# Kernel optimization log

Hardware: AMD Instinct MI355X
Metric: run time of the kernel (lower is better)

## Reference

```python
import math
import jax, jax.numpy as jnp
import numpy as np

B, T, S, C, E = 16, 1024, 1024, 1024, 1024
NORM_C = 0.5


def setup_inputs() -> dict:
    key = jax.random.key(0)
    ks = jax.random.split(key, 9)
    return {
        "x": jax.random.normal(ks[0], (B, T, C), dtype=jnp.float32),
        "target_embedding": jax.random.normal(ks[1], (B, T, E), dtype=jnp.float32),
        "enc_keys": jax.random.normal(ks[2], (B, E, S), dtype=jnp.float32),      # encoder_out[0]
        "enc_values": jax.random.normal(ks[3], (B, S, E), dtype=jnp.float32),    # encoder_out[1]
        "encoder_padding_mask": jax.random.randint(ks[4], (B, S), 0, 2).astype(bool),
        "w_in": jax.random.normal(ks[5], (E, C), dtype=jnp.float32) / np.sqrt(C),
        "b_in": jnp.zeros((E,), dtype=jnp.float32),
        "w_out": jax.random.normal(ks[6], (C, E), dtype=jnp.float32) / np.sqrt(E),
        "b_out": jnp.zeros((C,), dtype=jnp.float32),
    }


def reference(x, target_embedding, enc_keys, enc_values, encoder_padding_mask,
              w_in, b_in, w_out, b_out):
    scale = jnp.float32(math.sqrt(NORM_C))
    residual = x
    # in_projection + target embedding, rescale
    h = (jnp.einsum("btc,ec->bte", x, w_in) + b_in + target_embedding) * scale
    # attention scores: bmm with keys [B,E,S]
    scores = jnp.einsum("bte,bes->bts", h, enc_keys)
    neg_inf = jnp.float32(float("-inf"))
    scores = jnp.where(encoder_padding_mask[:, None, :], neg_inf, scores)
    attn_scores = jax.nn.softmax(scores, axis=-1)
    # weighted sum of values
    ctx = jnp.einsum("bts,bse->bte", attn_scores, enc_values)
    # data-dependent rescale: multiply by sqrt(valid token count)
    s = jnp.float32(S) - jnp.sum(encoder_padding_mask.astype(ctx.dtype), axis=1, keepdims=True)  # [B,1]
    s = s[:, :, None]  # [B,1,1]
    ctx = ctx * (s * jax.lax.rsqrt(s))
    out = (jnp.einsum("bte,ce->btc", ctx, w_out) + b_out + residual) * scale
    return (out, attn_scores)
```

## Files before the change

kernel.cpp:

```cpp
#include <hip/hip_runtime.h>


#define SCALE_F 0.70710678118654752440f

constexpr int BB = 16, TT = 1024, SS = 1024, CC = 1024, EE = 1024;

typedef float    f32x4 __attribute__((ext_vector_type(4)));
typedef _Float16 f16x8 __attribute__((ext_vector_type(8)));
typedef _Float16 f16x4 __attribute__((ext_vector_type(4)));

__device__ __forceinline__ void gload_lds16(const _Float16* g, _Float16* l) {
  __builtin_amdgcn_global_load_lds((const __attribute__((address_space(1))) void*)g,
                                   (__attribute__((address_space(3))) void*)l,
                                   16, 0, 0);
}

__global__ __launch_bounds__(256) void cvt_f16(const float* __restrict__ s,
                                               _Float16* __restrict__ d, long n) {
  long i = ((long)blockIdx.x * 256 + threadIdx.x) * 8;
  if (i >= n) return;
  f32x4 a = *(const f32x4*)(s + i);
  f32x4 b = *(const f32x4*)(s + i + 4);
  f16x8 h;
  h[0]=(_Float16)a[0]; h[1]=(_Float16)a[1]; h[2]=(_Float16)a[2]; h[3]=(_Float16)a[3];
  h[4]=(_Float16)b[0]; h[5]=(_Float16)b[1]; h[6]=(_Float16)b[2]; h[7]=(_Float16)b[3];
  *(f16x8*)(d + i) = h;
}

__global__ __launch_bounds__(256) void transpose_cvt(const float* __restrict__ src,
                                                     _Float16* __restrict__ dst,
                                                     int R, int Cc) {
  __shared__ float tile[64][65];
  const int b = blockIdx.z;
  const int r0 = blockIdx.y * 64, c0 = blockIdx.x * 64;
  const int t = threadIdx.x;
  const int tr = t >> 4, tc4 = (t & 15) * 4;
  const float* s = src + (size_t)b * R * Cc;
#pragma unroll
  for (int i = 0; i < 4; ++i) {
    f32x4 v = *(const f32x4*)(s + (size_t)(r0 + i * 16 + tr) * Cc + c0 + tc4);
    tile[i * 16 + tr][tc4 + 0] = v[0]; tile[i * 16 + tr][tc4 + 1] = v[1];
    tile[i * 16 + tr][tc4 + 2] = v[2]; tile[i * 16 + tr][tc4 + 3] = v[3];
  }
  __syncthreads();
  _Float16* d = dst + (size_t)b * Cc * R;
#pragma unroll
  for (int j = 0; j < 4; ++j) {
    const int cl = j * 16 + tr;
    f16x4 h;
    h[0] = (_Float16)tile[tc4 + 0][cl]; h[1] = (_Float16)tile[tc4 + 1][cl];
    h[2] = (_Float16)tile[tc4 + 2][cl]; h[3] = (_Float16)tile[tc4 + 3][cl];
    *(f16x4*)(d + (size_t)(c0 + cl) * R + r0 + tc4) = h;
  }
}

__global__ __launch_bounds__(256) void mask_prep(const unsigned char* __restrict__ mraw,
                                                 float* __restrict__ maskneg,
                                                 float* __restrict__ sscale) {
  const int b = blockIdx.x, t = threadIdx.x;
  __shared__ int bytemode_sh, cnt_sh;
  if (t == 0) { bytemode_sh = 0; cnt_sh = 0; }
  __syncthreads();
  const unsigned int* mu = (const unsigned int*)mraw;
  int local = 0;
  for (int i = t; i < (BB * SS) / 4; i += 256) {
    unsigned int v = mu[i];
    if (v != 0u && v != 1u && v != 0x3f800000u) local = 1;
  }
  if (local) atomicOr(&bytemode_sh, 1);
  __syncthreads();
  const int bytemode = bytemode_sh;
  int cnt = 0;
  for (int s = t; s < SS; s += 256) {
    int m = bytemode ? (mraw[b * SS + s] != 0) : (mu[b * SS + s] != 0u);
    maskneg[b * SS + s] = m ? -__builtin_inff() : 0.0f;
    cnt += m;
  }
#pragma unroll
  for (int o = 32; o; o >>= 1) cnt += __shfl_down(cnt, o);
  if ((t & 63) == 0) atomicAdd(&cnt_sh, cnt);
  __syncthreads();
  if (t == 0) {
    float sv = (float)SS - (float)cnt_sh;
    sscale[b] = sv * rsqrtf(sv);
  }
}

template <int EPI>
__global__ __launch_bounds__(256, 4)
void gemm_hp(const _Float16* __restrict__ A, const _Float16* __restrict__ Bmat,
             long aStride, long bStride, long oStride,
             int M, int N, int K,
             void* __restrict__ outp,
             const float* __restrict__ bias,
             const void* __restrict__ addmat,
             const float* __restrict__ extra) {
  __shared__ __attribute__((aligned(16))) _Float16 smem[2][8192];

  const int t = threadIdx.x;
  const int lane = t & 63;
  const int wid = t >> 6;
  const int wr = wid >> 1, wc = wid & 1;
  const int z = blockIdx.z;
  const int lo = lane & 15, hi = lane >> 4;
  const int nt = K >> 5;

  const int gx = gridDim.x;
  const int fblk = blockIdx.x + blockIdx.y * gx;
  const int q = (gx * gridDim.y) >> 3;
  const int wg = (fblk & 7) * q + (fblk >> 3);
  const long rowBase = (long)(wg / gx) * 128;
  const long colBase = (long)(wg % gx) * 128;

  const _Float16* Ag = A + (size_t)z * aStride + rowBase * K;
  const _Float16* Bg = Bmat + (size_t)z * bStride + colBase * K;

  const int sP = t >> 3;
  const int sl = (t & 7) ^ (sP & 7);
  const int sh64 = (sl >> 2) * 64;
  const int sc8 = (sl & 3) * 8;

  f32x4 acc[4][4] = {};

  auto stage = [&](int buf, int u) {
    _Float16* base = &smem[buf][0];
    const size_t k0 = (size_t)u * 32 + sc8;
#pragma unroll
    for (int op = 0; op < 2; ++op) {
      const _Float16* g = op ? Bg : Ag;
#pragma unroll
      for (int i = 0; i < 2; ++i) {
        const int gRow = 32 * i + sP + sh64;
        gload_lds16(g + (size_t)gRow * K + k0,
                    base + op * 4096 + i * 2048 + t * 8);
      }
    }
  };

  stage(0, 0);
  asm volatile("s_waitcnt vmcnt(0)" ::: "memory");
  __syncthreads();

  const int aslot = ((4 * wr + hi) ^ (lo & 7)) << 3;
  const int bslot = ((4 * wc + hi) ^ (lo & 7)) << 3;

  for (int u = 0; u < nt; ++u) {
    if (u + 1 < nt) stage((u + 1) & 1, u + 1);
    const _Float16* As = &smem[u & 1][0];
    const _Float16* Bs = &smem[u & 1][4096];
    f16x8 a[4], b[4];
#pragma unroll
    for (int m = 0; m < 4; ++m)
      a[m] = *(const f16x8*)&As[(m * 16 + lo) * 64 + aslot];
#pragma unroll
    for (int n = 0; n < 4; ++n)
      b[n] = *(const f16x8*)&Bs[(n * 16 + lo) * 64 + bslot];
#pragma unroll
    for (int m = 0; m < 4; ++m)
#pragma unroll
      for (int n = 0; n < 4; ++n)
        acc[m][n] = __builtin_amdgcn_mfma_f32_16x16x32_f16(a[m], b[n],
                                                           acc[m][n], 0, 0, 0);
    __syncthreads();
  }

  constexpr int EPS = 68;
  const int fr = lane & 15;
  const int fq = (lane >> 4) * 4;
  const int er = lane >> 2;
  const int ec = (lane & 3) * 16;
  const long gc0 = colBase + wc * 64 + ec;
  float* ep = (float*)&smem[0][0] + wid * (16 * EPS);

  f32x4 biasv[4], maskv[4], av[4];
  float sc = 0.f;
  auto load_add = [&](long gr) {
    if constexpr (EPI == 1) {
      const float* am = (const float*)addmat;
#pragma unroll
      for (int i = 0; i < 4; ++i) av[i] = *(const f32x4*)&am[gr * N + gc0 + i * 4];
    } else if constexpr (EPI == 5) {
      const _Float16* am = (const _Float16*)addmat;
      f16x8 h0 = *(const f16x8*)&am[gr * N + gc0];
      f16x8 h1 = *(const f16x8*)&am[gr * N + gc0 + 8];
#pragma unroll
      for (int i = 0; i < 4; ++i) {
        const f16x8& hh = i < 2 ? h0 : h1;
        const int o = (i & 1) * 4;
        av[i][0] = (float)hh[o]; av[i][1] = (float)hh[o + 1];
        av[i][2] = (float)hh[o + 2]; av[i][3] = (float)hh[o + 3];
      }
    }
  };
  if constexpr (EPI == 1 || EPI == 5) {
#pragma unroll
    for (int i = 0; i < 4; ++i) biasv[i] = *(const f32x4*)&bias[gc0 + i * 4];
    load_add(rowBase + wr * 64 + er);
  }
  if constexpr (EPI == 2) {
#pragma unroll
    for (int i = 0; i < 4; ++i)
      maskv[i] = *(const f32x4*)&((const float*)addmat)[(size_t)z * N + gc0 + i * 4];
  }
  if constexpr (EPI == 3) sc = extra[z];

#pragma unroll
  for (int mf = 0; mf < 4; ++mf) {
#pragma unroll
    for (int n = 0; n < 4; ++n)
#pragma unroll
      for (int j = 0; j < 4; ++j)
        ep[(fq + j) * EPS + n * 16 + fr] = acc[mf][n][j];
    __syncthreads();
    const long gr = rowBase + wr * 64 + mf * 16 + er;
    f32x4 r[4];
#pragma unroll
    for (int i = 0; i < 4; ++i) r[i] = *(const f32x4*)&ep[er * EPS + ec + i * 4];
    f32x4 a_cur[4];
    if constexpr (EPI == 1 || EPI == 5) {
#pragma unroll
      for (int i = 0; i < 4; ++i) a_cur[i] = av[i];
      if (mf < 3) load_add(gr + 16);
    }
    if constexpr (EPI == 1) {
      _Float16* o = (_Float16*)outp + gr * N + gc0;
#pragma unroll
      for (int g = 0; g < 2; ++g) {
        f32x4 v0 = (r[2 * g] + biasv[2 * g] + a_cur[2 * g]) * SCALE_F;
        f32x4 v1 = (r[2 * g + 1] + biasv[2 * g + 1] + a_cur[2 * g + 1]) * SCALE_F;
        f16x8 h;
        h[0]=(_Float16)v0[0]; h[1]=(_Float16)v0[1]; h[2]=(_Float16)v0[2]; h[3]=(_Float16)v0[3];
        h[4]=(_Float16)v1[0]; h[5]=(_Float16)v1[1]; h[6]=(_Float16)v1[2]; h[7]=(_Float16)v1[3];
        *(f16x8*)(o + g * 8) = h;
      }
    } else if constexpr (EPI == 2) {
      float* o = (float*)outp + (size_t)z * oStride + gr * N + gc0;
#pragma unroll
      for (int i = 0; i < 4; ++i) *(f32x4*)(o + i * 4) = r[i] + maskv[i];
    } else if constexpr (EPI == 3) {
      _Float16* o = (_Float16*)outp + (size_t)z * oStride + gr * N + gc0;
#pragma unroll
      for (int g = 0; g < 2; ++g) {
        f32x4 v0 = r[2 * g] * sc;
        f32x4 v1 = r[2 * g + 1] * sc;
        f16x8 h;
        h[0]=(_Float16)v0[0]; h[1]=(_Float16)v0[1]; h[2]=(_Float16)v0[2]; h[3]=(_Float16)v0[3];
        h[4]=(_Float16)v1[0]; h[5]=(_Float16)v1[1]; h[6]=(_Float16)v1[2]; h[7]=(_Float16)v1[3];
        *(f16x8*)(o + g * 8) = h;
      }
    } else {
      float* o = (float*)outp + gr * N + gc0;
#pragma unroll
      for (int i = 0; i < 4; ++i)
        *(f32x4*)(o + i * 4) = (r[i] + biasv[i] + a_cur[i]) * SCALE_F;
    }
    __syncthreads();
  }
}

__global__ __launch_bounds__(256) void softmax_k(float* __restrict__ attn,
                                                 _Float16* __restrict__ attn16) {
  const size_t row = blockIdx.x;
  float* p = attn + row * SS;
  const int t = threadIdx.x;
  f32x4 v = *(const f32x4*)(p + t * 4);
  __shared__ float red[8];
  float m = fmaxf(fmaxf(v[0], v[1]), fmaxf(v[2], v[3]));
#pragma unroll
  for (int o = 32; o; o >>= 1) m = fmaxf(m, __shfl_xor(m, o));
  if (!(t & 63)) red[t >> 6] = m;
  __syncthreads();
  m = fmaxf(fmaxf(red[0], red[1]), fmaxf(red[2], red[3]));
  f32x4 e;
  e[0] = __expf(v[0] - m); e[1] = __expf(v[1] - m);
  e[2] = __expf(v[2] - m); e[3] = __expf(v[3] - m);
  float s = e[0] + e[1] + e[2] + e[3];
#pragma unroll
  for (int o = 32; o; o >>= 1) s += __shfl_xor(s, o);
  if (!(t & 63)) red[4 + (t >> 6)] = s;
  __syncthreads();
  s = red[4] + red[5] + red[6] + red[7];
  const float inv = 1.0f / s;
  f32x4 o4; o4[0]=e[0]*inv; o4[1]=e[1]*inv; o4[2]=e[2]*inv; o4[3]=e[3]*inv;
  *(f32x4*)(p + t * 4) = o4;
  f16x4 h; h[0]=(_Float16)o4[0]; h[1]=(_Float16)o4[1];
  h[2]=(_Float16)o4[2]; h[3]=(_Float16)o4[3];
  *(f16x4*)(attn16 + row * SS + t * 4) = h;
}

extern "C" void kernel_launch(void* const* d_in, const int* in_sizes, int n_in,
                              void* d_out, int out_size, void* d_ws, size_t ws_size,
                              hipStream_t stream) {
  const float* x     = (const float*)d_in[0];
  const float* te    = (const float*)d_in[1];
  const float* keys  = (const float*)d_in[2];
  const float* vals  = (const float*)d_in[3];
  const void*  mask  = d_in[4];
  const float* w_in  = (const float*)d_in[5];
  const float* b_in  = (const float*)d_in[6];
  const float* w_out = (const float*)d_in[7];
  const float* b_out = (const float*)d_in[8];

  char* ws = (char*)d_ws;
  const size_t MB32 = 33554432;
  _Float16* buf0   = (_Float16*)(ws);
  _Float16* buf1   = (_Float16*)(ws + MB32);
  _Float16* keysT  = (_Float16*)(ws + 2 * MB32);
  _Float16* valsT  = (_Float16*)(ws + 3 * MB32);
  _Float16* win16  = (_Float16*)(ws + 4 * MB32);
  _Float16* wout16 = (_Float16*)(ws + 4 * MB32 + 2097152);
  float*    maskneg= (float*)   (ws + 4 * MB32 + 2 * 2097152);
  float*    sscale = (float*)   (ws + 4 * MB32 + 2 * 2097152 + 65536);

  float* out_main = (float*)d_out;
  float* attn_out = (float*)d_out + (size_t)BB * TT * CC;

  cvt_f16<<<dim3(16777216 / 2048), 256, 0, stream>>>(x, buf0, 16777216);
  cvt_f16<<<dim3(1048576 / 2048), 256, 0, stream>>>(w_in, win16, 1048576);
  cvt_f16<<<dim3(1048576 / 2048), 256, 0, stream>>>(w_out, wout16, 1048576);
  transpose_cvt<<<dim3(SS / 64, EE / 64, BB), 256, 0, stream>>>(keys, keysT, EE, SS);
  transpose_cvt<<<dim3(EE / 64, SS / 64, BB), 256, 0, stream>>>(vals, valsT, SS, EE);
  mask_prep<<<dim3(BB), 256, 0, stream>>>((const unsigned char*)mask, maskneg, sscale);

  gemm_hp<1><<<dim3(EE / 128, (BB * TT) / 128, 1), 256, 0, stream>>>(
      buf0, win16, 0, 0, 0, BB * TT, EE, CC, buf1, b_in, te, nullptr);
  gemm_hp<2><<<dim3(SS / 128, TT / 128, BB), 256, 0, stream>>>(
      buf1, keysT, (long)TT * EE, (long)SS * EE, (long)TT * SS,
      TT, SS, EE, attn_out, nullptr, maskneg, nullptr);
  softmax_k<<<dim3(BB * TT), 256, 0, stream>>>(attn_out, buf1);
  gemm_hp<3><<<dim3(EE / 128, TT / 128, BB), 256, 0, stream>>>(
      buf1, valsT, (long)TT * SS, (long)EE * SS, (long)TT * EE,
      TT, EE, SS, keysT, nullptr, nullptr, sscale);
  gemm_hp<5><<<dim3(CC / 128, (BB * TT) / 128, 1), 256, 0, stream>>>(
      keysT, wout16, 0, 0, 0, BB * TT, CC, EE, out_main, b_out, buf0, nullptr);
}
```

Measured before the change: 338.6 us.

## Load B operand directly into registers and deepen K tile to 64

The GEMM kernel now stages only the A tile through LDS (via global_load_lds) and loads B fragments straight from global memory into registers, prefetching the next K step into a second register set. The K tile doubles from 32 to 64, halving the number of barriers, and occupancy hint drops from 4 to 2 blocks per SM. This removes LDS traffic and space for B, at the cost of more VGPRs, uncoalesced per-lane global reads of B and possibly lower occupancy.

```diff
diff --git a/kernel.cpp b/kernel.cpp
--- a/kernel.cpp
+++ b/kernel.cpp
@@ -87,15 +87,16 @@
 }
 
 template <int EPI>
-__global__ __launch_bounds__(256, 4)
-void gemm_hp(const _Float16* __restrict__ A, const _Float16* __restrict__ Bmat,
+__global__ __launch_bounds__(256, 2)
+void gemm_bd(const _Float16* __restrict__ A, const _Float16* __restrict__ Bmat,
              long aStride, long bStride, long oStride,
              int M, int N, int K,
              void* __restrict__ outp,
              const float* __restrict__ bias,
              const void* __restrict__ addmat,
              const float* __restrict__ extra) {
-  __shared__ __attribute__((aligned(16))) _Float16 smem[2][8192];
+  constexpr int BM = 128, BK = 64;
+  __shared__ __attribute__((aligned(16))) _Float16 As[2][BM * BK];
 
   const int t = threadIdx.x;
   const int lane = t & 63;
@@ -103,7 +104,8 @@
   const int wr = wid >> 1, wc = wid & 1;
   const int z = blockIdx.z;
   const int lo = lane & 15, hi = lane >> 4;
-  const int nt = K >> 5;
+  const int sx = lo & 7;
+  const int nt = K >> 6;
 
   const int gx = gridDim.x;
   const int fblk = blockIdx.x + blockIdx.y * gx;
@@ -115,53 +117,69 @@
   const _Float16* Ag = A + (size_t)z * aStride + rowBase * K;
   const _Float16* Bg = Bmat + (size_t)z * bStride + colBase * K;
 
-  const int sP = t >> 3;
-  const int sl = (t & 7) ^ (sP & 7);
-  const int sh64 = (sl >> 2) * 64;
-  const int sc8 = (sl & 3) * 8;
+  const int srow = t >> 3;
+  const int scol = 8 * ((t & 7) ^ (srow & 7));
 
   f32x4 acc[4][4] = {};
-
-  auto stage = [&](int buf, int u) {
-    _Float16* base = &smem[buf][0];
-    const size_t k0 = (size_t)u * 32 + sc8;
-#pragma unroll
-    for (int op = 0; op < 2; ++op) {
-      const _Float16* g = op ? Bg : Ag;
-#pragma unroll
-      for (int i = 0; i < 2; ++i) {
-        const int gRow = 32 * i + sP + sh64;
-        gload_lds16(g + (size_t)gRow * K + k0,
-                    base + op * 4096 + i * 2048 + t * 8);
-      }
-    }
+  f16x8 bcur[2][4], bnxt[2][4];
+
+  const _Float16* bp[2][4];
+#pragma unroll
+  for (int ks = 0; ks < 2; ++ks)
+#pragma unroll
+    for (int n = 0; n < 4; ++n)
+      bp[ks][n] = Bg + (size_t)(wc * 64 + n * 16 + lo) * K + ks * 32 + hi * 8;
+
+  auto stageA = [&](int buf, int u) {
+#pragma unroll
+    for (int qq = 0; qq < 4; ++qq)
+      gload_lds16(Ag + (size_t)(qq * 32 + srow) * K + u * 64 + scol,
+                  &As[buf][(qq * 256 + t) * 8]);
   };
 
-  stage(0, 0);
+  stageA(0, 0);
+#pragma unroll
+  for (int ks = 0; ks < 2; ++ks)
+#pragma unroll
+    for (int n = 0; n < 4; ++n)
+      bcur[ks][n] = *(const f16x8*)(bp[ks][n]);
   asm volatile("s_waitcnt vmcnt(0)" ::: "memory");
   __syncthreads();
 
-  const int aslot = ((4 * wr + hi) ^ (lo & 7)) << 3;
-  const int bslot = ((4 * wc + hi) ^ (lo & 7)) << 3;
-
   for (int u = 0; u < nt; ++u) {
-    if (u + 1 < nt) stage((u + 1) & 1, u + 1);
-    const _Float16* As = &smem[u & 1][0];
-    const _Float16* Bs = &smem[u & 1][4096];
-    f16x8 a[4], b[4];
-#pragma unroll
-    for (int m = 0; m < 4; ++m)
-      a[m] = *(const f16x8*)&As[(m * 16 + lo) * 64 + aslot];
-#pragma unroll
-    for (int n = 0; n < 4; ++n)
-      b[n] = *(const f16x8*)&Bs[(n * 16 + lo) * 64 + bslot];
-#pragma unroll
-    for (int m = 0; m < 4; ++m)
-#pragma unroll
-      for (int n = 0; n < 4; ++n)
-        acc[m][n] = __builtin_amdgcn_mfma_f32_16x16x32_f16(a[m], b[n],
-                                                           acc[m][n], 0, 0, 0);
+    if (u + 1 < nt) {
+      stageA((u + 1) & 1, u + 1);
+#pragma unroll
+      for (int ks = 0; ks < 2; ++ks)
+#pragma unroll
+        for (int n = 0; n < 4; ++n)
+          bnxt[ks][n] = *(const f16x8*)(bp[ks][n] + (u + 1) * 64);
+    }
+    const _Float16* Asb = &As[u & 1][0];
+    f16x8 a[2][4];
+#pragma unroll
+    for (int ks = 0; ks < 2; ++ks) {
+      const int slot = (ks * 4 + hi) ^ sx;
+#pragma unroll
+      for (int m = 0; m < 4; ++m)
+        a[ks][m] = *(const f16x8*)&Asb[(wr * 64 + m * 16 + lo) * 64 + slot * 8];
+    }
+#pragma unroll
+    for (int ks = 0; ks < 2; ++ks)
+#pragma unroll
+      for (int m = 0; m < 4; ++m)
+#pragma unroll
+        for (int n = 0; n < 4; ++n)
+          acc[m][n] = __builtin_amdgcn_mfma_f32_16x16x32_f16(
+              a[ks][m], bcur[ks][n], acc[m][n], 0, 0, 0);
     __syncthreads();
+    if (u + 1 < nt) {
+#pragma unroll
+      for (int ks = 0; ks < 2; ++ks)
+#pragma unroll
+        for (int n = 0; n < 4; ++n)
+          bcur[ks][n] = bnxt[ks][n];
+    }
   }
 
   constexpr int EPS = 68;
@@ -170,7 +188,7 @@
   const int er = lane >> 2;
   const int ec = (lane & 3) * 16;
   const long gc0 = colBase + wc * 64 + ec;
-  float* ep = (float*)&smem[0][0] + wid * (16 * EPS);
+  float* ep = (float*)&As[0][0] + wid * (16 * EPS);
 
   f32x4 biasv[4], maskv[4], av[4];
   float sc = 0.f;
@@ -322,15 +340,15 @@
   transpose_cvt<<<dim3(EE / 64, SS / 64, BB), 256, 0, stream>>>(vals, valsT, SS, EE);
   mask_prep<<<dim3(BB), 256, 0, stream>>>((const unsigned char*)mask, maskneg, sscale);
 
-  gemm_hp<1><<<dim3(EE / 128, (BB * TT) / 128, 1), 256, 0, stream>>>(
+  gemm_bd<1><<<dim3(EE / 128, (BB * TT) / 128, 1), 256, 0, stream>>>(
       buf0, win16, 0, 0, 0, BB * TT, EE, CC, buf1, b_in, te, nullptr);
-  gemm_hp<2><<<dim3(SS / 128, TT / 128, BB), 256, 0, stream>>>(
+  gemm_bd<2><<<dim3(SS / 128, TT / 128, BB), 256, 0, stream>>>(
       buf1, keysT, (long)TT * EE, (long)SS * EE, (long)TT * SS,
       TT, SS, EE, attn_out, nullptr, maskneg, nullptr);
   softmax_k<<<dim3(BB * TT), 256, 0, stream>>>(attn_out, buf1);
-  gemm_hp<3><<<dim3(EE / 128, TT / 128, BB), 256, 0, stream>>>(
+  gemm_bd<3><<<dim3(EE / 128, TT / 128, BB), 256, 0, stream>>>(
       buf1, valsT, (long)TT * SS, (long)EE * SS, (long)TT * EE,
       TT, EE, SS, keysT, nullptr, nullptr, sscale);
-  gemm_hp<5><<<dim3(CC / 128, (BB * TT) / 128, 1), 256, 0, stream>>>(
+  gemm_bd<5><<<dim3(CC / 128, (BB * TT) / 128, 1), 256, 0, stream>>>(
       keysT, wout16, 0, 0, 0, BB * TT, CC, EE, out_main, b_out, buf0, nullptr);
 }
```

Measured after the change: 450.2 us. +33.0%, slower.

## Restructure GEMM into 256x128 tiles with triple-buffered K=64 LDS pipeline

Applied to the files above, without the earlier changes.

Replaces the 128x128, 256-thread, double-buffered GEMM with a 512-thread kernel that computes 256x128 tiles. It uses a 3-stage LDS ring with K=64 per stage, prefetching two stages ahead. LDS reads are issued as inline-asm ds_read_b128 with explicit lgkmcnt/vmcnt waits, split into two halves so MFMAs on the first half overlap the remaining reads, and s_setprio is raised around the MFMA blocks. The aim is to hide global-load latency and raise MFMA utilisation, at the cost of 144KB LDS per block and fragile hand-managed waits and swizzles.

```diff
diff --git a/kernel.cpp b/kernel.cpp
--- a/kernel.cpp
+++ b/kernel.cpp
@@ -14,6 +14,12 @@
                                    (__attribute__((address_space(3))) void*)l,
                                    16, 0, 0);
 }
+
+#define VMCNT(N) asm volatile("s_waitcnt vmcnt(" #N ")" ::: "memory")
+#define LGKM(N)  asm volatile("s_waitcnt lgkmcnt(" #N ")" ::: "memory")
+#define SBAR()   asm volatile("s_barrier" ::: "memory")
+#define DSR(dst, a, off) \
+  asm volatile("ds_read_b128 %0, %1 offset:" #off : "=v"(dst) : "v"(a))
 
 __global__ __launch_bounds__(256) void cvt_f16(const float* __restrict__ s,
                                                _Float16* __restrict__ d, long n) {
@@ -87,90 +93,114 @@
 }
 
 template <int EPI>
-__global__ __launch_bounds__(256, 4)
-void gemm_hp(const _Float16* __restrict__ A, const _Float16* __restrict__ Bmat,
+__global__ __launch_bounds__(512, 2)
+void gemm_t3(const _Float16* __restrict__ A, const _Float16* __restrict__ Bmat,
              long aStride, long bStride, long oStride,
              int M, int N, int K,
              void* __restrict__ outp,
              const float* __restrict__ bias,
              const void* __restrict__ addmat,
              const float* __restrict__ extra) {
-  __shared__ __attribute__((aligned(16))) _Float16 smem[2][8192];
+  __shared__ __attribute__((aligned(16))) _Float16 smem[73728];
 
   const int t = threadIdx.x;
   const int lane = t & 63;
   const int wid = t >> 6;
-  const int wr = wid >> 1, wc = wid & 1;
+  const int wm = wid >> 1, wn = wid & 1;
   const int z = blockIdx.z;
   const int lo = lane & 15, hi = lane >> 4;
-  const int nt = K >> 5;
+  const int nt = K >> 6;
 
   const int gx = gridDim.x;
   const int fblk = blockIdx.x + blockIdx.y * gx;
   const int q = (gx * gridDim.y) >> 3;
   const int wg = (fblk & 7) * q + (fblk >> 3);
-  const long rowBase = (long)(wg / gx) * 128;
+  const long rowBase = (long)(wg / gx) * 256;
   const long colBase = (long)(wg % gx) * 128;
 
   const _Float16* Ag = A + (size_t)z * aStride + rowBase * K;
   const _Float16* Bg = Bmat + (size_t)z * bStride + colBase * K;
 
-  const int sP = t >> 3;
-  const int sl = (t & 7) ^ (sP & 7);
-  const int sh64 = (sl >> 2) * 64;
-  const int sc8 = (sl & 3) * 8;
+  const int strow = t >> 2;
+  const int stchunk = (t & 3) ^ ((t >> 3) & 3);
 
   f32x4 acc[4][4] = {};
 
-  auto stage = [&](int buf, int u) {
-    _Float16* base = &smem[buf][0];
-    const size_t k0 = (size_t)u * 32 + sc8;
-#pragma unroll
-    for (int op = 0; op < 2; ++op) {
-      const _Float16* g = op ? Bg : Ag;
-#pragma unroll
-      for (int i = 0; i < 2; ++i) {
-        const int gRow = 32 * i + sP + sh64;
-        gload_lds16(g + (size_t)gRow * K + k0,
-                    base + op * 4096 + i * 2048 + t * 8);
-      }
-    }
+  auto stg6 = [&](int U, int b3) {
+    _Float16* ab = &smem[b3 * 16384];
+    _Float16* bb = &smem[49152 + b3 * 8192];
+    const size_t ko = (size_t)U * 64 + stchunk * 8;
+    gload_lds16(Ag + (size_t)strow * K + ko,             ab + t * 8);
+    gload_lds16(Ag + (size_t)(strow + 128) * K + ko,     ab + 4096 + t * 8);
+    gload_lds16(Ag + (size_t)strow * K + ko + 32,        ab + 8192 + t * 8);
+    gload_lds16(Ag + (size_t)(strow + 128) * K + ko + 32, ab + 12288 + t * 8);
+    gload_lds16(Bg + (size_t)strow * K + ko,             bb + t * 8);
+    gload_lds16(Bg + (size_t)strow * K + ko + 32,        bb + 4096 + t * 8);
   };
 
-  stage(0, 0);
-  asm volatile("s_waitcnt vmcnt(0)" ::: "memory");
-  __syncthreads();
-
-  const int aslot = ((4 * wr + hi) ^ (lo & 7)) << 3;
-  const int bslot = ((4 * wc + hi) ^ (lo & 7)) << 3;
-
+  const int lds0 = (int)(size_t)&smem[0];
+  const int slotx = (hi ^ ((lo >> 1) & 3)) << 4;
+  const int abase = lds0 + wm * 4096 + lo * 64 + slotx;
+  const int bbase = lds0 + 98304 + wn * 4096 + lo * 64 + slotx;
+
+  stg6(0, 0);
+  stg6(1, 1);
+  VMCNT(6);
+  SBAR();
+
+  int bufR = 0, bufS = 2;
   for (int u = 0; u < nt; ++u) {
-    if (u + 1 < nt) stage((u + 1) & 1, u + 1);
-    const _Float16* As = &smem[u & 1][0];
-    const _Float16* Bs = &smem[u & 1][4096];
-    f16x8 a[4], b[4];
-#pragma unroll
-    for (int m = 0; m < 4; ++m)
-      a[m] = *(const f16x8*)&As[(m * 16 + lo) * 64 + aslot];
-#pragma unroll
-    for (int n = 0; n < 4; ++n)
-      b[n] = *(const f16x8*)&Bs[(n * 16 + lo) * 64 + bslot];
-#pragma unroll
-    for (int m = 0; m < 4; ++m)
-#pragma unroll
-      for (int n = 0; n < 4; ++n)
-        acc[m][n] = __builtin_amdgcn_mfma_f32_16x16x32_f16(a[m], b[n],
-                                                           acc[m][n], 0, 0, 0);
-    __syncthreads();
-  }
+    const int aad0 = abase + bufR * 32768;
+    const int aad1 = aad0 + 16384;
+    const int bad0 = bbase + bufR * 16384;
+    const int bad1 = bad0 + 8192;
+    f16x8 a0[4], b0[4], a1[4], b1[4];
+    DSR(a0[0], aad0, 0); DSR(a0[1], aad0, 1024);
+    DSR(a0[2], aad0, 2048); DSR(a0[3], aad0, 3072);
+    DSR(b0[0], bad0, 0); DSR(b0[1], bad0, 1024);
+    DSR(b0[2], bad0, 2048); DSR(b0[3], bad0, 3072);
+    DSR(a1[0], aad1, 0); DSR(a1[1], aad1, 1024);
+    DSR(a1[2], aad1, 2048); DSR(a1[3], aad1, 3072);
+    DSR(b1[0], bad1, 0); DSR(b1[1], bad1, 1024);
+    DSR(b1[2], bad1, 2048); DSR(b1[3], bad1, 3072);
+    if (u + 2 < nt) stg6(u + 2, bufS);
+    LGKM(8);
+    __builtin_amdgcn_sched_barrier(0);
+    __builtin_amdgcn_s_setprio(1);
+#pragma unroll
+    for (int mi = 0; mi < 4; ++mi)
+#pragma unroll
+      for (int ni = 0; ni < 4; ++ni)
+        acc[mi][ni] = __builtin_amdgcn_mfma_f32_16x16x32_f16(a0[mi], b0[ni],
+                                                             acc[mi][ni], 0, 0, 0);
+    __builtin_amdgcn_s_setprio(0);
+    LGKM(0);
+    __builtin_amdgcn_sched_barrier(0);
+    __builtin_amdgcn_s_setprio(1);
+#pragma unroll
+    for (int mi = 0; mi < 4; ++mi)
+#pragma unroll
+      for (int ni = 0; ni < 4; ++ni)
+        acc[mi][ni] = __builtin_amdgcn_mfma_f32_16x16x32_f16(a1[mi], b1[ni],
+                                                             acc[mi][ni], 0, 0, 0);
+    __builtin_amdgcn_s_setprio(0);
+    if (u < nt - 2)       { VMCNT(6); }
+    else if (u == nt - 2) { VMCNT(0); }
+    SBAR();
+    bufR = (bufR == 2) ? 0 : bufR + 1;
+    bufS = (bufS == 2) ? 0 : bufS + 1;
+  }
+
+  LGKM(0);
+  __syncthreads();
 
   constexpr int EPS = 68;
   const int fr = lane & 15;
   const int fq = (lane >> 4) * 4;
   const int er = lane >> 2;
   const int ec = (lane & 3) * 16;
-  const long gc0 = colBase + wc * 64 + ec;
-  float* ep = (float*)&smem[0][0] + wid * (16 * EPS);
+  const long gc0 = colBase + wn * 64 + ec;
+  float* ep = (float*)smem + wid * (16 * EPS);
 
   f32x4 biasv[4], maskv[4], av[4];
   float sc = 0.f;
@@ -195,7 +225,7 @@
   if constexpr (EPI == 1 || EPI == 5) {
 #pragma unroll
     for (int i = 0; i < 4; ++i) biasv[i] = *(const f32x4*)&bias[gc0 + i * 4];
-    load_add(rowBase + wr * 64 + er);
+    load_add(rowBase + wm * 64 + er);
   }
   if constexpr (EPI == 2) {
 #pragma unroll
@@ -212,7 +242,7 @@
       for (int j = 0; j < 4; ++j)
         ep[(fq + j) * EPS + n * 16 + fr] = acc[mf][n][j];
     __syncthreads();
-    const long gr = rowBase + wr * 64 + mf * 16 + er;
+    const long gr = rowBase + wm * 64 + mf * 16 + er;
     f32x4 r[4];
 #pragma unroll
     for (int i = 0; i < 4; ++i) r[i] = *(const f32x4*)&ep[er * EPS + ec + i * 4];
@@ -322,15 +352,15 @@
   transpose_cvt<<<dim3(EE / 64, SS / 64, BB), 256, 0, stream>>>(vals, valsT, SS, EE);
   mask_prep<<<dim3(BB), 256, 0, stream>>>((const unsigned char*)mask, maskneg, sscale);
 
-  gemm_hp<1><<<dim3(EE / 128, (BB * TT) / 128, 1), 256, 0, stream>>>(
+  gemm_t3<1><<<dim3(EE / 128, (BB * TT) / 256, 1), 512, 0, stream>>>(
       buf0, win16, 0, 0, 0, BB * TT, EE, CC, buf1, b_in, te, nullptr);
-  gemm_hp<2><<<dim3(SS / 128, TT / 128, BB), 256, 0, stream>>>(
+  gemm_t3<2><<<dim3(SS / 128, TT / 256, BB), 512, 0, stream>>>(
       buf1, keysT, (long)TT * EE, (long)SS * EE, (long)TT * SS,
       TT, SS, EE, attn_out, nullptr, maskneg, nullptr);
   softmax_k<<<dim3(BB * TT), 256, 0, stream>>>(attn_out, buf1);
-  gemm_hp<3><<<dim3(EE / 128, TT / 128, BB), 256, 0, stream>>>(
+  gemm_t3<3><<<dim3(EE / 128, TT / 256, BB), 512, 0, stream>>>(
       buf1, valsT, (long)TT * SS, (long)EE * SS, (long)TT * EE,
       TT, EE, SS, keysT, nullptr, nullptr, sscale);
-  gemm_hp<5><<<dim3(CC / 128, (BB * TT) / 128, 1), 256, 0, stream>>>(
+  gemm_t3<5><<<dim3(CC / 128, (BB * TT) / 256, 1), 512, 0, stream>>>(
       keysT, wout16, 0, 0, 0, BB * TT, CC, EE, out_main, b_out, buf0, nullptr);
 }
```

Result: faster. 327.4 us (-3.3%).
